# Kernel tuning notes

Hardware: AMD Instinct MI355X
Metric: run time of the kernel (lower is better)

The kernel has to match this reference:

```python
import jax, jax.numpy as jnp
import numpy as np

VOCAB = 128000
EMBED = 256
BATCH = 64
BLOCK = 2048


def setup_inputs() -> dict:
    key = jax.random.key(0)
    k_idx, k_emb = jax.random.split(key)
    idx = jax.random.randint(k_idx, (BATCH, BLOCK), 0, VOCAB, dtype=jnp.int64 if jax.config.read('jax_enable_x64') else jnp.int32)
    embedding = jax.random.normal(k_emb, (VOCAB, EMBED), dtype=jnp.float32)
    return {"idx": idx, "embedding": embedding}


def reference(idx, embedding):
    # one_hot(idx) @ embedding is mathematically a row gather
    logits = embedding[idx]                      # [B, T, E]
    # original unstable exp-normalize (softmax without max subtraction)
    counts = jnp.exp(logits)
    probs = counts / jnp.sum(counts, axis=-1, keepdims=True)
    return (logits, probs)
```

## Files before the change

### kernel.cpp

```cpp
#include <hip/hip_runtime.h>

#define VOCAB 128000
#define EMBED 256
#define BATCH 64
#define TBLOCK 2048
#define ROWS (BATCH * TBLOCK)

__global__ __launch_bounds__(256) void embed_expnorm_kernel(
    const int* __restrict__ idx,
    const float* __restrict__ emb,
    float* __restrict__ logits,
    float* __restrict__ probs)
{
    const int gtid = blockIdx.x * blockDim.x + threadIdx.x;
    const int wave = gtid >> 6;
    const int lane = gtid & 63;

    if (wave >= ROWS) return;

    const int row = idx[wave];

    const float4* rowp = reinterpret_cast<const float4*>(emb + (long long)row * EMBED);
    const float4 v = rowp[lane];

    float4 e;
    e.x = __expf(v.x);
    e.y = __expf(v.y);
    e.z = __expf(v.z);
    e.w = __expf(v.w);

    float s = (e.x + e.y) + (e.z + e.w);
    #pragma unroll
    for (int m = 1; m < 64; m <<= 1)
        s += __shfl_xor(s, m, 64);

    const float inv = 1.0f / s;

    float4 p;
    p.x = e.x * inv;
    p.y = e.y * inv;
    p.z = e.z * inv;
    p.w = e.w * inv;

    const long long off = (long long)wave * (EMBED / 4) + lane;
    reinterpret_cast<float4*>(logits)[off] = v;
    reinterpret_cast<float4*>(probs)[off]  = p;
}

extern "C" void kernel_launch(void* const* d_in, const int* in_sizes, int n_in,
                              void* d_out, int out_size, void* d_ws, size_t ws_size,
                              hipStream_t stream) {
    const int*   idx = (const int*)d_in[0];
    const float* emb = (const float*)d_in[1];

    float* out    = (float*)d_out;
    float* logits = out;
    float* probs  = out + (long long)ROWS * EMBED;

    const int blocks = ROWS / 4;
    embed_expnorm_kernel<<<blocks, 256, 0, stream>>>(idx, emb, logits, probs);
}
```

Measured before the change: 356.3 us.

## Process eight rows per wave with batched loads and nontemporal stores

Each wavefront now handles eight gathered embedding rows instead of one. It loads the indices as two int4 vectors and issues all eight row loads before any compute, which raises memory-level parallelism. The shuffle reductions are interleaved across rows, exp is recomputed instead of kept in registers, and outputs are written with nontemporal stores to avoid polluting the cache. The grid shrinks by a factor of eight, which trades occupancy and wave count for more loads in flight per wave.

```diff
diff --git a/kernel.cpp b/kernel.cpp
--- a/kernel.cpp
+++ b/kernel.cpp
@@ -6,45 +6,69 @@
 #define TBLOCK 2048
 #define ROWS (BATCH * TBLOCK)
 
+#define RPW 8
+#define WPB 4
+#define ROWS_PER_BLOCK (RPW * WPB)
+
+typedef float v4f __attribute__((ext_vector_type(4)));
+
 __global__ __launch_bounds__(256) void embed_expnorm_kernel(
     const int* __restrict__ idx,
     const float* __restrict__ emb,
     float* __restrict__ logits,
     float* __restrict__ probs)
 {
-    const int gtid = blockIdx.x * blockDim.x + threadIdx.x;
-    const int wave = gtid >> 6;
-    const int lane = gtid & 63;
+    const int lane = threadIdx.x & 63;
+    const int wid  = blockIdx.x * WPB + (threadIdx.x >> 6);
+    const long long rowbase = (long long)wid * RPW;
 
-    if (wave >= ROWS) return;
+    const int4* ip = reinterpret_cast<const int4*>(idx + rowbase);
+    const int4 i0 = ip[0];
+    const int4 i1 = ip[1];
+    int rows[RPW];
+    rows[0] = i0.x; rows[1] = i0.y; rows[2] = i0.z; rows[3] = i0.w;
+    rows[4] = i1.x; rows[5] = i1.y; rows[6] = i1.z; rows[7] = i1.w;
 
-    const int row = idx[wave];
+    v4f v[RPW];
+    #pragma unroll
+    for (int r = 0; r < RPW; ++r) {
+        const v4f* rowp =
+            reinterpret_cast<const v4f*>(emb + (long long)rows[r] * EMBED);
+        v[r] = rowp[lane];
+    }
 
-    const float4* rowp = reinterpret_cast<const float4*>(emb + (long long)row * EMBED);
-    const float4 v = rowp[lane];
+    float s[RPW];
+    #pragma unroll
+    for (int r = 0; r < RPW; ++r) {
+        const float ex = __expf(v[r].x);
+        const float ey = __expf(v[r].y);
+        const float ez = __expf(v[r].z);
+        const float ew = __expf(v[r].w);
+        s[r] = (ex + ey) + (ez + ew);
+    }
 
-    float4 e;
-    e.x = __expf(v.x);
-    e.y = __expf(v.y);
-    e.z = __expf(v.z);
-    e.w = __expf(v.w);
+    #pragma unroll
+    for (int m = 1; m < 64; m <<= 1) {
+        #pragma unroll
+        for (int r = 0; r < RPW; ++r)
+            s[r] += __shfl_xor(s[r], m, 64);
+    }
 
-    float s = (e.x + e.y) + (e.z + e.w);
+    v4f* lp = reinterpret_cast<v4f*>(logits);
+    v4f* pp = reinterpret_cast<v4f*>(probs);
     #pragma unroll
-    for (int m = 1; m < 64; m <<= 1)
-        s += __shfl_xor(s, m, 64);
+    for (int r = 0; r < RPW; ++r) {
+        const float inv = 1.0f / s[r];
+        v4f p;
+        p.x = __expf(v[r].x) * inv;
+        p.y = __expf(v[r].y) * inv;
+        p.z = __expf(v[r].z) * inv;
+        p.w = __expf(v[r].w) * inv;
 
-    const float inv = 1.0f / s;
-
-    float4 p;
-    p.x = e.x * inv;
-    p.y = e.y * inv;
-    p.z = e.z * inv;
-    p.w = e.w * inv;
-
-    const long long off = (long long)wave * (EMBED / 4) + lane;
-    reinterpret_cast<float4*>(logits)[off] = v;
-    reinterpret_cast<float4*>(probs)[off]  = p;
+        const long long off = (rowbase + r) * (EMBED / 4) + lane;
+        __builtin_nontemporal_store(v[r], lp + off);
+        __builtin_nontemporal_store(p,    pp + off);
+    }
 }
 
 extern "C" void kernel_launch(void* const* d_in, const int* in_sizes, int n_in,
@@ -57,6 +81,6 @@
     float* logits = out;
     float* probs  = out + (long long)ROWS * EMBED;
 
-    const int blocks = ROWS / 4;
+    const int blocks = ROWS / ROWS_PER_BLOCK;
     embed_expnorm_kernel<<<blocks, 256, 0, stream>>>(idx, emb, logits, probs);
 }
```

Measured after the change: 356.4 us. Within noise of the previous version (+0.0%).
